# Optimization experiments

Measured on AMD Instinct MI355X. Metric: run time of the kernel, lower is better.

Reference implementation:

```python
import jax, jax.numpy as jnp
import numpy as np

POSE_IDS = np.array([0, 4, 8, 12, 16])
BN_EPS = 1e-5


def setup_inputs() -> dict:
    key = jax.random.key(0)
    ks = jax.random.split(key, 8)
    N, C, H, W = 64, 2048, 24, 12
    P, Cl = 5, 256
    Cm = C + P * Cl  # 3328
    return {
        "x": jax.random.normal(ks[0], (N, C, H, W), jnp.float32),
        "poses": jax.random.uniform(ks[1], (N, 17, 4), jnp.float32),
        "local_w": jax.random.normal(ks[2], (P, Cl, C), jnp.float32) * 0.02,
        "local_b": jnp.zeros((P, Cl), jnp.float32),
        "local_gamma": jnp.ones((P, Cl), jnp.float32),
        "local_beta": jnp.zeros((P, Cl), jnp.float32),
        "local_mean": jax.random.normal(ks[3], (P, Cl), jnp.float32) * 0.1,
        "local_var": jax.random.uniform(ks[4], (P, Cl), jnp.float32, 0.5, 1.5),
        "merge_w": jax.random.normal(ks[5], (C, Cm), jnp.float32) * 0.02,
        "merge_b": jnp.zeros((C,), jnp.float32),
        "merge_gamma": jnp.ones((C,), jnp.float32),
        "merge_beta": jnp.zeros((C,), jnp.float32),
        "merge_mean": jax.random.normal(ks[6], (C,), jnp.float32) * 0.1,
        "merge_var": jax.random.uniform(ks[7], (C,), jnp.float32, 0.5, 1.5),
    }


def reference(x, poses, local_w, local_b, local_gamma, local_beta, local_mean,
              local_var, merge_w, merge_b, merge_gamma, merge_beta, merge_mean,
              merge_var):
    N, C, H, W = x.shape
    kp = poses[:, jnp.asarray(POSE_IDS), :]  # [N,P,4]
    # box = [left, top, w, h]; clamp to [0, 0.75]; scale whole box by confidence
    half = jnp.full_like(kp[..., 0], 0.5)
    box = jnp.stack([kp[..., 0] - 0.25, kp[..., 1] - 0.25, half, half], axis=-1)
    box = jnp.clip(box, 0.0, 0.75) * kp[..., 2:3]
    # integer ROI bounds on the feature grid (round-half-to-even like torch)
    xs = jnp.maximum(0, jnp.round(W * box[..., 0])).astype(jnp.int32)          # [N,P]
    xe = jnp.minimum(W - 1, jnp.round(W * (box[..., 0] + box[..., 2]))).astype(jnp.int32)
    ys = jnp.maximum(0, jnp.round(H * box[..., 1])).astype(jnp.int32)
    ye = jnp.minimum(H - 1, jnp.round(H * (box[..., 1] + box[..., 3]))).astype(jnp.int32)
    rows = jnp.arange(H)
    cols = jnp.arange(W)
    mh = (rows[None, None, :] >= ys[..., None]) & (rows[None, None, :] < ye[..., None])  # [N,P,H]
    mw = (cols[None, None, :] >= xs[..., None]) & (cols[None, None, :] < xe[..., None])  # [N,P,W]
    mask = (mh[..., :, None] & mw[..., None, :]).astype(x.dtype)  # [N,P,H,W]
    # masked average pool over the ROI (single pass over x)
    sums = jnp.einsum('nchw,nphw->npc', x, mask)
    area = ((ye - ys) * (xe - xs)).astype(x.dtype)
    avg = sums / jnp.where(area > 0, area, 1.0)[..., None]  # [N,P,C], 0 for empty ROIs
    # per-part 1x1 conv + BN(eval) + ReLU -> [N,P,Cl]
    loc = jnp.einsum('npc,pkc->npk', avg, local_w) + local_b[None]
    loc = (loc - local_mean[None]) * (local_gamma[None] / jnp.sqrt(local_var[None] + BN_EPS)) + local_beta[None]
    loc = jax.nn.relu(loc)
    # global max pool -> [N,C]
    gfeat = x.max(axis=(2, 3))
    cat = jnp.concatenate([loc.reshape(N, -1), gfeat], axis=1)  # [N, P*Cl + C]
    # merge 1x1 conv + BN(eval) + ReLU
    y = cat @ merge_w.T + merge_b
    y = (y - merge_mean) * (merge_gamma / jnp.sqrt(merge_var + BN_EPS)) + merge_beta
    y = jax.nn.relu(y)
    # F.normalize(p=2, dim=1)
    norm = jnp.linalg.norm(y, axis=1, keepdims=True)
    return y / jnp.maximum(norm, 1e-12)
```

## Files before the change

### kernel.cpp

```cpp
#include <hip/hip_runtime.h>

#define N_   64
#define C_   2048
#define HW_  288
#define P_   5
#define CM_  3328
#define LOC_ 1280
#define SEGC 8
#define SEGM 13

#define WPITCH 72

typedef __attribute__((ext_vector_type(8))) short bf16x8;
typedef __attribute__((ext_vector_type(4))) float f32x4;

__device__ __forceinline__ unsigned short f2bf(float f) {
  unsigned u = __float_as_uint(f);
  u = (u + 0x7FFFu + ((u >> 16) & 1u)) >> 16;
  return (unsigned short)u;
}
__device__ __forceinline__ unsigned pack2(float lo, float hi) {
  return (unsigned)f2bf(lo) | ((unsigned)f2bf(hi) << 16);
}

__device__ __forceinline__ void load16_lds(const float4* g, void* l) {
  __builtin_amdgcn_global_load_lds(
      (const __attribute__((address_space(1))) void*)g,
      (__attribute__((address_space(3))) void*)l, 16, 0, 0);
}

__global__ __launch_bounds__(256) void kB(const float* __restrict__ x,
    const float* __restrict__ poses,
    unsigned short* __restrict__ avgB, unsigned short* __restrict__ catB) {
  __shared__ float lds[2][256 * 36];
  const int t  = threadIdx.x;
  const int n  = blockIdx.x >> 3;
  const int cb = (blockIdx.x & 7) << 8;
  const int chbase = n * C_ + cb;

  unsigned MH[P_], MW[P_];
  float INV[P_];
  const float* kpn = poses + (size_t)n * 68;
#pragma unroll
  for (int p = 0; p < P_; ++p) {
    const float* kp = kpn + 16 * p;
    float px = kp[0], py = kp[1], z = kp[2];
    float bx = fminf(fmaxf(px - 0.25f, 0.f), 0.75f) * z;
    float by = fminf(fmaxf(py - 0.25f, 0.f), 0.75f) * z;
    float bw = 0.5f * z;
    float bh = 0.5f * z;
    int xs = (int)fmaxf(0.f,  rintf(12.f * bx));
    int xe = (int)fminf(11.f, rintf(12.f * (bx + bw)));
    int ys = (int)fmaxf(0.f,  rintf(24.f * by));
    int ye = (int)fminf(23.f, rintf(24.f * (by + bh)));
    MH[p] = ((1u << ye) - 1u) & ~((1u << ys) - 1u);
    MW[p] = ((1u << xe) - 1u) & ~((1u << xs) - 1u);
    int area = (ye - ys) * (xe - xs);
    INV[p] = area > 0 ? 1.f / (float)area : 1.f;
  }

  const float4* x4 = (const float4*)x;
  unsigned goff[9];
#pragma unroll
  for (int k = 0; k < 9; ++k) {
    unsigned slot = k * 256u + (unsigned)t;
    unsigned ch = slot / 9u;
    unsigned j  = slot - 9u * ch;
    goff[k] = (unsigned)(chbase + ch) * 72u + j;
  }
  const unsigned wbase = ((unsigned)t & 192u) * 16u;

  float s[P_] = {0.f, 0.f, 0.f, 0.f, 0.f};
  float mx = -3.402823466e+38f;

  {
    char* base = (char*)&lds[0][0];
#pragma unroll
    for (int k = 0; k < 9; ++k)
      load16_lds(x4 + goff[k], base + (k * 4096u + wbase));
  }
  asm volatile("s_waitcnt vmcnt(0)" ::: "memory");
  __syncthreads();

  for (int ci = 0; ci < 8; ++ci) {
    if (ci + 1 < 8) {
      char* base = (char*)&lds[(ci + 1) & 1][0];
#pragma unroll
      for (int k = 0; k < 9; ++k)
        load16_lds(x4 + goff[k] + (ci + 1) * 9, base + (k * 4096u + wbase));
    }
    const float* row = &lds[ci & 1][t * 36];
#pragma unroll
    for (int r = 0; r < 3; ++r) {
      int h = 3 * ci + r;
      float4 a = *(const float4*)(row + r * 12 + 0);
      float4 b = *(const float4*)(row + r * 12 + 4);
      float4 c = *(const float4*)(row + r * 12 + 8);
      float m1 = fmaxf(fmaxf(a.x, a.y), fmaxf(a.z, a.w));
      float m2 = fmaxf(fmaxf(b.x, b.y), fmaxf(b.z, b.w));
      float m3 = fmaxf(fmaxf(c.x, c.y), fmaxf(c.z, c.w));
      mx = fmaxf(mx, fmaxf(m1, fmaxf(m2, m3)));
#pragma unroll
      for (int p = 0; p < P_; ++p) {
        unsigned cm = ((MH[p] >> h) & 1u) ? MW[p] : 0u;
        if (cm) {
          float t0 = ((cm & 0x001u) ? a.x : 0.f) + ((cm & 0x002u) ? a.y : 0.f);
          float t1 = ((cm & 0x004u) ? a.z : 0.f) + ((cm & 0x008u) ? a.w : 0.f);
          float t2 = ((cm & 0x010u) ? b.x : 0.f) + ((cm & 0x020u) ? b.y : 0.f);
          float t3 = ((cm & 0x040u) ? b.z : 0.f) + ((cm & 0x080u) ? b.w : 0.f);
          float t4 = ((cm & 0x100u) ? c.x : 0.f) + ((cm & 0x200u) ? c.y : 0.f);
          float t5 = ((cm & 0x400u) ? c.z : 0.f) + ((cm & 0x800u) ? c.w : 0.f);
          s[p] += ((t0 + t1) + (t2 + t3)) + (t4 + t5);
        }
      }
    }
    if (ci + 1 < 8) {
      asm volatile("s_waitcnt vmcnt(0)" ::: "memory");
      __syncthreads();
    }
  }

  int c = cb + t;
  catB[(size_t)n * CM_ + LOC_ + c] = f2bf(mx);
#pragma unroll
  for (int p = 0; p < P_; ++p)
    avgB[((size_t)n * 5 + p) * C_ + c] = f2bf(s[p] * INV[p]);
}

__device__ __forceinline__ void mfma_seg(const uint4* __restrict__ aRow,
                                         const float4* __restrict__ wRow,
                                         unsigned short* As, unsigned short* Ws,
                                         f32x4 acc[4]) {
  const int t  = threadIdx.x;
  const int kq = t & 3;
  const int row = t >> 2;
  const int w  = t >> 6;
  const int l  = t & 63;
  unsigned short* aw = &As[row * WPITCH + kq * 16];
  unsigned short* ww = &Ws[row * WPITCH + kq * 16];
  const int arow16 = (16 * w + (l & 15)) * WPITCH + (l >> 4) * 8;
  const int brow16 = (l & 15) * WPITCH + (l >> 4) * 8;
  uint4 a0 = aRow[0], a1 = aRow[1];
  float4 w0 = wRow[0], w1 = wRow[1], w2 = wRow[2], w3 = wRow[3];
  for (int g = 0; g < 4; ++g) {
    uint4 pw0, pw1;
    pw0.x = pack2(w0.x, w0.y); pw0.y = pack2(w0.z, w0.w);
    pw0.z = pack2(w1.x, w1.y); pw0.w = pack2(w1.z, w1.w);
    pw1.x = pack2(w2.x, w2.y); pw1.y = pack2(w2.z, w2.w);
    pw1.z = pack2(w3.x, w3.y); pw1.w = pack2(w3.z, w3.w);
    if (g) __syncthreads();
    *(uint4*)aw = a0; *(uint4*)(aw + 8) = a1;
    *(uint4*)ww = pw0; *(uint4*)(ww + 8) = pw1;
    if (g < 3) {
      a0 = aRow[g * 8 + 8];  a1 = aRow[g * 8 + 9];
      w0 = wRow[g * 16 + 16]; w1 = wRow[g * 16 + 17];
      w2 = wRow[g * 16 + 18]; w3 = wRow[g * 16 + 19];
    }
    __syncthreads();
#pragma unroll
    for (int s = 0; s < 2; ++s) {
      bf16x8 af = *(const bf16x8*)&As[arow16 + s * 32];
#pragma unroll
      for (int jm = 0; jm < 4; ++jm) {
        bf16x8 bf = *(const bf16x8*)&Ws[jm * 16 * WPITCH + brow16 + s * 32];
        acc[jm] = __builtin_amdgcn_mfma_f32_16x16x32_bf16(af, bf, acc[jm], 0, 0, 0);
      }
    }
  }
}

__global__ __launch_bounds__(256) void kC(const unsigned short* __restrict__ avgB,
                                          const float* __restrict__ local_w,
                                          float* __restrict__ locP) {
  __shared__ unsigned short As[64 * WPITCH];
  __shared__ unsigned short Ws[64 * WPITCH];
  int b  = blockIdx.x;
  int p  = b >> 5;
  int kt = (b >> 3) & 3;
  int sg = b & 7;
  const int t = threadIdx.x, row = t >> 2, kq = t & 3, w = t >> 6, l = t & 63;
  const uint4*  aRow = (const uint4*)avgB + ((size_t)row * 5 + p) * 256 + sg * 32 + kq * 2;
  const float4* wRow = (const float4*)(local_w + ((size_t)p * 256 + kt * 64 + row) * C_
                                       + sg * 256 + kq * 16);
  f32x4 acc[4] = {{0,0,0,0},{0,0,0,0},{0,0,0,0},{0,0,0,0}};
  mfma_seg(aRow, wRow, As, Ws, acc);
  float* outp = locP + (size_t)sg * (N_ * LOC_);
#pragma unroll
  for (int jm = 0; jm < 4; ++jm)
#pragma unroll
    for (int r = 0; r < 4; ++r)
      outp[(size_t)(16 * w + (l >> 4) * 4 + r) * LOC_ + p * 256 + kt * 64 + jm * 16 + (l & 15)]
        = acc[jm][r];
}

__global__ __launch_bounds__(256) void kC2(const float* __restrict__ locP,
    const float* __restrict__ lb, const float* __restrict__ lg, const float* __restrict__ lbe,
    const float* __restrict__ lm, const float* __restrict__ lv,
    unsigned short* __restrict__ catB) {
  int i = blockIdx.x * 256 + threadIdx.x;
  int n = i / LOC_;
  int q = i - n * LOC_;
  float s = 0.f;
#pragma unroll
  for (int sg = 0; sg < SEGC; ++sg) s += locP[(size_t)sg * (N_ * LOC_) + i];
  float sc = lg[q] / sqrtf(lv[q] + 1e-5f);
  float v = (s + lb[q] - lm[q]) * sc + lbe[q];
  catB[(size_t)n * CM_ + q] = f2bf(fmaxf(v, 0.f));
}

__global__ __launch_bounds__(256) void kD(const unsigned short* __restrict__ catB,
                                          const float* __restrict__ merge_w,
                                          float* __restrict__ mrgP) {
  __shared__ unsigned short As[64 * WPITCH];
  __shared__ unsigned short Ws[64 * WPITCH];
  int b  = blockIdx.x;
  int jt = b / SEGM;
  int sg = b - jt * SEGM;
  const int t = threadIdx.x, row = t >> 2, kq = t & 3, w = t >> 6, l = t & 63;
  const uint4*  aRow = (const uint4*)catB + (size_t)row * 416 + sg * 32 + kq * 2;
  const float4* wRow = (const float4*)(merge_w + (size_t)(jt * 64 + row) * CM_
                                       + sg * 256 + kq * 16);
  f32x4 acc[4] = {{0,0,0,0},{0,0,0,0},{0,0,0,0},{0,0,0,0}};
  mfma_seg(aRow, wRow, As, Ws, acc);
  float* outp = mrgP + (size_t)sg * (N_ * C_);
#pragma unroll
  for (int jm = 0; jm < 4; ++jm)
#pragma unroll
    for (int r = 0; r < 4; ++r)
      outp[(size_t)(16 * w + (l >> 4) * 4 + r) * C_ + jt * 64 + jm * 16 + (l & 15)]
        = acc[jm][r];
}

__global__ __launch_bounds__(256) void kE1(const float* __restrict__ mrgP,
    const float* __restrict__ mb, const float* __restrict__ mg, const float* __restrict__ mbe,
    const float* __restrict__ mm, const float* __restrict__ mv,
    float* __restrict__ z, float* __restrict__ part) {
  int nb = blockIdx.x;
  int n = nb >> 3, t = threadIdx.x;
  int j = ((nb & 7) << 8) + t;
  float y = 0.f;
#pragma unroll
  for (int sg = 0; sg < SEGM; ++sg) y += mrgP[(size_t)sg * (N_ * C_) + (size_t)n * C_ + j];
  float sc = mg[j] / sqrtf(mv[j] + 1e-5f);
  float v = (y + mb[j] - mm[j]) * sc + mbe[j];
  v = fmaxf(v, 0.f);
  z[(size_t)n * C_ + j] = v;
  float ss = v * v;
#pragma unroll
  for (int off = 32; off; off >>= 1) ss += __shfl_xor(ss, off, 64);
  __shared__ float red[4];
  if ((t & 63) == 0) red[t >> 6] = ss;
  __syncthreads();
  if (t == 0) part[nb] = (red[0] + red[1]) + (red[2] + red[3]);
}

__global__ __launch_bounds__(256) void kE2(const float* __restrict__ z,
    const float* __restrict__ part, float* __restrict__ out) {
  int nb = blockIdx.x;
  int n = nb >> 3, t = threadIdx.x;
  int j = ((nb & 7) << 8) + t;
  const float* pp = part + n * 8;
  float tot = ((pp[0] + pp[1]) + (pp[2] + pp[3])) + ((pp[4] + pp[5]) + (pp[6] + pp[7]));
  float inv = 1.f / fmaxf(sqrtf(tot), 1e-12f);
  out[(size_t)n * C_ + j] = z[(size_t)n * C_ + j] * inv;
}

extern "C" void kernel_launch(void* const* d_in, const int* in_sizes, int n_in,
                              void* d_out, int out_size, void* d_ws, size_t ws_size,
                              hipStream_t stream) {
  const float* x          = (const float*)d_in[0];
  const float* poses      = (const float*)d_in[1];
  const float* local_w    = (const float*)d_in[2];
  const float* local_b    = (const float*)d_in[3];
  const float* local_g    = (const float*)d_in[4];
  const float* local_be   = (const float*)d_in[5];
  const float* local_m    = (const float*)d_in[6];
  const float* local_v    = (const float*)d_in[7];
  const float* merge_w    = (const float*)d_in[8];
  const float* merge_b    = (const float*)d_in[9];
  const float* merge_g    = (const float*)d_in[10];
  const float* merge_be   = (const float*)d_in[11];
  const float* merge_m    = (const float*)d_in[12];
  const float* merge_v    = (const float*)d_in[13];

  char* ws = (char*)d_ws;
  unsigned short* catB = (unsigned short*)ws;
  unsigned short* avgB = (unsigned short*)(ws + 425984);
  float* locP = (float*)(ws + 1736704);
  float* mrgP = (float*)(ws + 4358144);
  float* z    = (float*)(ws + 1736704);
  float* part = (float*)(ws + 2260992);

  kB<<<512, 256, 0, stream>>>(x, poses, avgB, catB);
  kC<<<20 * SEGC, 256, 0, stream>>>(avgB, local_w, locP);
  kC2<<<(N_ * LOC_) / 256, 256, 0, stream>>>(locP, local_b, local_g, local_be,
                                             local_m, local_v, catB);
  kD<<<32 * SEGM, 256, 0, stream>>>(catB, merge_w, mrgP);
  kE1<<<512, 256, 0, stream>>>(mrgP, merge_b, merge_g, merge_be, merge_m, merge_v,
                               z, part);
  kE2<<<512, 256, 0, stream>>>(z, part, (float*)d_out);
}
```

Before: 282.3 us.

## Fuse BN/ReLU and L2-normalize via inter-block flags; double-buffer GEMM prefetch

```diff
diff --git a/kernel.cpp b/kernel.cpp
--- a/kernel.cpp
+++ b/kernel.cpp
@@ -127,6 +127,7 @@
     avgB[((size_t)n * 5 + p) * C_ + c] = f2bf(s[p] * INV[p]);
 }
 
+template<int NG>
 __device__ __forceinline__ void mfma_seg(const uint4* __restrict__ aRow,
                                          const float4* __restrict__ wRow,
                                          unsigned short* As, unsigned short* Ws,
@@ -140,21 +141,31 @@
   unsigned short* ww = &Ws[row * WPITCH + kq * 16];
   const int arow16 = (16 * w + (l & 15)) * WPITCH + (l >> 4) * 8;
   const int brow16 = (l & 15) * WPITCH + (l >> 4) * 8;
-  uint4 a0 = aRow[0], a1 = aRow[1];
-  float4 w0 = wRow[0], w1 = wRow[1], w2 = wRow[2], w3 = wRow[3];
-  for (int g = 0; g < 4; ++g) {
+  uint4 pa[2][2];
+  float4 pw[2][4];
+  pa[0][0] = aRow[0]; pa[0][1] = aRow[1];
+  pw[0][0] = wRow[0]; pw[0][1] = wRow[1]; pw[0][2] = wRow[2]; pw[0][3] = wRow[3];
+  if (NG > 1) {
+    pa[1][0] = aRow[8];  pa[1][1] = aRow[9];
+    pw[1][0] = wRow[16]; pw[1][1] = wRow[17];
+    pw[1][2] = wRow[18]; pw[1][3] = wRow[19];
+  }
+#pragma unroll
+  for (int g = 0; g < NG; ++g) {
+    const int sl = g & 1;
     uint4 pw0, pw1;
-    pw0.x = pack2(w0.x, w0.y); pw0.y = pack2(w0.z, w0.w);
-    pw0.z = pack2(w1.x, w1.y); pw0.w = pack2(w1.z, w1.w);
-    pw1.x = pack2(w2.x, w2.y); pw1.y = pack2(w2.z, w2.w);
-    pw1.z = pack2(w3.x, w3.y); pw1.w = pack2(w3.z, w3.w);
+    pw0.x = pack2(pw[sl][0].x, pw[sl][0].y); pw0.y = pack2(pw[sl][0].z, pw[sl][0].w);
+    pw0.z = pack2(pw[sl][1].x, pw[sl][1].y); pw0.w = pack2(pw[sl][1].z, pw[sl][1].w);
+    pw1.x = pack2(pw[sl][2].x, pw[sl][2].y); pw1.y = pack2(pw[sl][2].z, pw[sl][2].w);
+    pw1.z = pack2(pw[sl][3].x, pw[sl][3].y); pw1.w = pack2(pw[sl][3].z, pw[sl][3].w);
+    uint4 a0 = pa[sl][0], a1 = pa[sl][1];
     if (g) __syncthreads();
     *(uint4*)aw = a0; *(uint4*)(aw + 8) = a1;
     *(uint4*)ww = pw0; *(uint4*)(ww + 8) = pw1;
-    if (g < 3) {
-      a0 = aRow[g * 8 + 8];  a1 = aRow[g * 8 + 9];
-      w0 = wRow[g * 16 + 16]; w1 = wRow[g * 16 + 17];
-      w2 = wRow[g * 16 + 18]; w3 = wRow[g * 16 + 19];
+    if (g + 2 < NG) {
+      pa[sl][0] = aRow[(g + 2) * 8];      pa[sl][1] = aRow[(g + 2) * 8 + 1];
+      pw[sl][0] = wRow[(g + 2) * 16];     pw[sl][1] = wRow[(g + 2) * 16 + 1];
+      pw[sl][2] = wRow[(g + 2) * 16 + 2]; pw[sl][3] = wRow[(g + 2) * 16 + 3];
     }
     __syncthreads();
 #pragma unroll
@@ -183,7 +194,7 @@
   const float4* wRow = (const float4*)(local_w + ((size_t)p * 256 + kt * 64 + row) * C_
                                        + sg * 256 + kq * 16);
   f32x4 acc[4] = {{0,0,0,0},{0,0,0,0},{0,0,0,0},{0,0,0,0}};
-  mfma_seg(aRow, wRow, As, Ws, acc);
+  mfma_seg<4>(aRow, wRow, As, Ws, acc);
   float* outp = locP + (size_t)sg * (N_ * LOC_);
 #pragma unroll
   for (int jm = 0; jm < 4; ++jm)
@@ -210,9 +221,11 @@
 
 __global__ __launch_bounds__(256) void kD(const unsigned short* __restrict__ catB,
                                           const float* __restrict__ merge_w,
-                                          float* __restrict__ mrgP) {
+                                          float* __restrict__ mrgP,
+                                          unsigned* __restrict__ flags) {
   __shared__ unsigned short As[64 * WPITCH];
   __shared__ unsigned short Ws[64 * WPITCH];
+  if (blockIdx.x == 0 && threadIdx.x < 256) flags[threadIdx.x] = 0u;
   int b  = blockIdx.x;
   int jt = b / SEGM;
   int sg = b - jt * SEGM;
@@ -221,7 +234,7 @@
   const float4* wRow = (const float4*)(merge_w + (size_t)(jt * 64 + row) * CM_
                                        + sg * 256 + kq * 16);
   f32x4 acc[4] = {{0,0,0,0},{0,0,0,0},{0,0,0,0},{0,0,0,0}};
-  mfma_seg(aRow, wRow, As, Ws, acc);
+  mfma_seg<4>(aRow, wRow, As, Ws, acc);
   float* outp = mrgP + (size_t)sg * (N_ * C_);
 #pragma unroll
   for (int jm = 0; jm < 4; ++jm)
@@ -231,38 +244,55 @@
         = acc[jm][r];
 }
 
-__global__ __launch_bounds__(256) void kE1(const float* __restrict__ mrgP,
-    const float* __restrict__ mb, const float* __restrict__ mg, const float* __restrict__ mbe,
-    const float* __restrict__ mm, const float* __restrict__ mv,
-    float* __restrict__ z, float* __restrict__ part) {
-  int nb = blockIdx.x;
-  int n = nb >> 3, t = threadIdx.x;
-  int j = ((nb & 7) << 8) + t;
-  float y = 0.f;
-#pragma unroll
-  for (int sg = 0; sg < SEGM; ++sg) y += mrgP[(size_t)sg * (N_ * C_) + (size_t)n * C_ + j];
-  float sc = mg[j] / sqrtf(mv[j] + 1e-5f);
-  float v = (y + mb[j] - mm[j]) * sc + mbe[j];
-  v = fmaxf(v, 0.f);
-  z[(size_t)n * C_ + j] = v;
-  float ss = v * v;
+__global__ __launch_bounds__(128) void kE(const float* __restrict__ mrgP,
+    const float* __restrict__ mb, const float* __restrict__ mg,
+    const float* __restrict__ mbe, const float* __restrict__ mm,
+    const float* __restrict__ mv, float* __restrict__ out,
+    float* __restrict__ part, unsigned* __restrict__ flags) {
+  const int b = blockIdx.x;
+  const int n = b >> 2, t = threadIdx.x;
+  const int j = ((b & 3) << 9) + (t << 2);
+  float4 y = {0.f, 0.f, 0.f, 0.f};
+#pragma unroll
+  for (int sg = 0; sg < SEGM; ++sg) {
+    float4 v = *(const float4*)&mrgP[(size_t)sg * (N_ * C_) + (size_t)n * C_ + j];
+    y.x += v.x; y.y += v.y; y.z += v.z; y.w += v.w;
+  }
+  float4 G  = *(const float4*)&mg[j];
+  float4 V  = *(const float4*)&mv[j];
+  float4 B  = *(const float4*)&mb[j];
+  float4 M  = *(const float4*)&mm[j];
+  float4 Be = *(const float4*)&mbe[j];
+  float z0 = fmaxf((y.x + B.x - M.x) * (G.x / sqrtf(V.x + 1e-5f)) + Be.x, 0.f);
+  float z1 = fmaxf((y.y + B.y - M.y) * (G.y / sqrtf(V.y + 1e-5f)) + Be.y, 0.f);
+  float z2 = fmaxf((y.z + B.z - M.z) * (G.z / sqrtf(V.z + 1e-5f)) + Be.z, 0.f);
+  float z3 = fmaxf((y.w + B.w - M.w) * (G.w / sqrtf(V.w + 1e-5f)) + Be.w, 0.f);
+  float ss = (z0 * z0 + z1 * z1) + (z2 * z2 + z3 * z3);
 #pragma unroll
   for (int off = 32; off; off >>= 1) ss += __shfl_xor(ss, off, 64);
-  __shared__ float red[4];
+  __shared__ float red[2];
+  __shared__ float tots;
   if ((t & 63) == 0) red[t >> 6] = ss;
   __syncthreads();
-  if (t == 0) part[nb] = (red[0] + red[1]) + (red[2] + red[3]);
-}
-
-__global__ __launch_bounds__(256) void kE2(const float* __restrict__ z,
-    const float* __restrict__ part, float* __restrict__ out) {
-  int nb = blockIdx.x;
-  int n = nb >> 3, t = threadIdx.x;
-  int j = ((nb & 7) << 8) + t;
-  const float* pp = part + n * 8;
-  float tot = ((pp[0] + pp[1]) + (pp[2] + pp[3])) + ((pp[4] + pp[5]) + (pp[6] + pp[7]));
-  float inv = 1.f / fmaxf(sqrtf(tot), 1e-12f);
-  out[(size_t)n * C_ + j] = z[(size_t)n * C_ + j] * inv;
+  if (t == 0) {
+    part[b] = red[0] + red[1];
+    __hip_atomic_store(&flags[b], 1u, __ATOMIC_RELEASE, __HIP_MEMORY_SCOPE_AGENT);
+    const int base = b & ~3;
+    float tot = 0.f;
+#pragma unroll
+    for (int k = 0; k < 4; ++k) {
+      while (__hip_atomic_load(&flags[base + k], __ATOMIC_ACQUIRE,
+                               __HIP_MEMORY_SCOPE_AGENT) == 0u) {}
+      tot += __hip_atomic_load(&part[base + k], __ATOMIC_RELAXED,
+                               __HIP_MEMORY_SCOPE_AGENT);
+    }
+    tots = tot;
+  }
+  __syncthreads();
+  float inv = 1.f / fmaxf(sqrtf(tots), 1e-12f);
+  float4 o;
+  o.x = z0 * inv; o.y = z1 * inv; o.z = z2 * inv; o.w = z3 * inv;
+  *(float4*)&out[(size_t)n * C_ + j] = o;
 }
 
 extern "C" void kernel_launch(void* const* d_in, const int* in_sizes, int n_in,
@@ -288,15 +318,14 @@
   unsigned short* avgB = (unsigned short*)(ws + 425984);
   float* locP = (float*)(ws + 1736704);
   float* mrgP = (float*)(ws + 4358144);
-  float* z    = (float*)(ws + 1736704);
-  float* part = (float*)(ws + 2260992);
+  float*    part  = (float*)(ws + 11173888);
+  unsigned* flags = (unsigned*)(ws + 11174912);
 
   kB<<<512, 256, 0, stream>>>(x, poses, avgB, catB);
   kC<<<20 * SEGC, 256, 0, stream>>>(avgB, local_w, locP);
   kC2<<<(N_ * LOC_) / 256, 256, 0, stream>>>(locP, local_b, local_g, local_be,
                                              local_m, local_v, catB);
-  kD<<<32 * SEGM, 256, 0, stream>>>(catB, merge_w, mrgP);
-  kE1<<<512, 256, 0, stream>>>(mrgP, merge_b, merge_g, merge_be, merge_m, merge_v,
-                               z, part);
-  kE2<<<512, 256, 0, stream>>>(z, part, (float*)d_out);
-}
+  kD<<<32 * SEGM, 256, 0, stream>>>(catB, merge_w, mrgP, flags);
+  kE<<<256, 128, 0, stream>>>(mrgP, merge_b, merge_g, merge_be, merge_m, merge_v,
+                              (float*)d_out, part, flags);
+}
```

New measurement: 292.2 us. +3.5%, slower.
